# Optimization experiments

Measured on AMD Instinct MI355X. Metric: run time of the kernel, lower is better.

Reference implementation:

```python
import jax, jax.numpy as jnp
import numpy as np
import math

N_EMBD = 1024
N_HEAD = 16
HEAD_DIM = N_EMBD // N_HEAD
B, T = 2, 2048
LORA_RANK = 16      # 8-bit setting
LORA_SCALE = 32.0 / 16.0  # alpha / rank
QMIN, QMAX = 0.0, 255.0   # 8-bit asymmetric


def round_ste(x):
    return x + jax.lax.stop_gradient(jnp.round(x) - x)


def fake_quant(x, scale, zero_point):
    # LearnableFakeQuantize, asymmetric 8-bit, straight-through round
    q = jnp.clip(round_ste(x / scale + zero_point), QMIN, QMAX)
    return (q - zero_point) * scale


def lora_linear(x, w, b, la, lb):
    # base linear + LoRA path (dropout disabled / eval)
    return x @ w + b + LORA_SCALE * ((x @ la) @ lb)


def setup_inputs() -> dict:
    key = jax.random.key(0)
    ks = jax.random.split(key, 10)
    std = 0.02
    hidden_states = jax.random.normal(ks[0], (B, T, N_EMBD), dtype=jnp.float32)
    w_attn = jax.random.normal(ks[1], (N_EMBD, 3 * N_EMBD), dtype=jnp.float32) * std
    b_attn = jnp.zeros((3 * N_EMBD,), dtype=jnp.float32)
    la_attn = jax.random.normal(ks[2], (N_EMBD, LORA_RANK), dtype=jnp.float32) * std
    lb_attn = jnp.zeros((LORA_RANK, 3 * N_EMBD), dtype=jnp.float32)
    w_proj = jax.random.normal(ks[3], (N_EMBD, N_EMBD), dtype=jnp.float32) * std
    b_proj = jnp.zeros((N_EMBD,), dtype=jnp.float32)
    la_proj = jax.random.normal(ks[4], (N_EMBD, LORA_RANK), dtype=jnp.float32) * std
    lb_proj = jnp.zeros((LORA_RANK, N_EMBD), dtype=jnp.float32)
    kv_scale = jnp.asarray(0.05, dtype=jnp.float32)
    kv_zero_point = jnp.asarray(128.0, dtype=jnp.float32)
    return {
        'hidden_states': hidden_states,
        'w_attn': w_attn, 'b_attn': b_attn, 'la_attn': la_attn, 'lb_attn': lb_attn,
        'w_proj': w_proj, 'b_proj': b_proj, 'la_proj': la_proj, 'lb_proj': lb_proj,
        'kv_scale': kv_scale, 'kv_zero_point': kv_zero_point,
    }


def reference(hidden_states, w_attn, b_attn, la_attn, lb_attn,
              w_proj, b_proj, la_proj, lb_proj, kv_scale, kv_zero_point):
    Bn, Tn, C = hidden_states.shape
    qkv = lora_linear(hidden_states, w_attn, b_attn, la_attn, lb_attn)
    q, k, v = jnp.split(qkv, 3, axis=2)
    # [B, T, C] -> [B, H, T, D]
    def to_heads(x):
        return x.reshape(Bn, Tn, N_HEAD, HEAD_DIM).transpose(0, 2, 1, 3)
    q, k, v = to_heads(q), to_heads(k), to_heads(v)
    k = fake_quant(k, kv_scale, kv_zero_point)
    v = fake_quant(v, kv_scale, kv_zero_point)
    scores = jnp.einsum('bhqd,bhkd->bhqk', q, k) / math.sqrt(HEAD_DIM)
    causal = jnp.tril(jnp.ones((Tn, Tn), dtype=bool))
    scores = jnp.where(causal, scores, -jnp.inf)
    attn = jax.nn.softmax(scores, axis=-1)
    out = jnp.einsum('bhqk,bhkd->bhqd', attn, v)
    out = out.transpose(0, 2, 1, 3).reshape(Bn, Tn, C)
    return lora_linear(out, w_proj, b_proj, la_proj, lb_proj)
```

## Files before the change

kernel.cpp:

```cpp
#include <hip/hip_runtime.h>
#include <hip/hip_bf16.h>
#include <math.h>

#define N_EMBD   1024
#define N_HEAD   16
#define HEAD_DIM 64
#define BATCH    2
#define TSEQ     2048
#define RANK     16
#define LORA_SCALE 2.0f
#define M_TOTAL  (BATCH * TSEQ)
#define C3       (3 * N_EMBD)

typedef unsigned short ushort_t;
typedef __attribute__((ext_vector_type(8))) short bf16x8;
typedef __attribute__((ext_vector_type(4))) float f32x4;

__device__ __forceinline__ float fake_quant(float x, float scale, float zp) {
    float q = rintf(x / scale + zp);
    q = fminf(fmaxf(q, 0.0f), 255.0f);
    return (q - zp) * scale;
}

__device__ __forceinline__ ushort_t bf16bits(float f) {
    union { __hip_bfloat16 h; ushort_t u; } c;
    c.h = __float2bfloat16(f);
    return c.u;
}

__device__ __forceinline__ float bfraw2f(ushort_t u) {
    union { unsigned int i; float f; } c; c.i = ((unsigned int)u) << 16; return c.f;
}

#define NB_LORA 1024
#define NB_TRA  3072
#define NB_TRP  1024
#define NB_CVT  4096

__device__ __forceinline__ void transpose_body(
        const float* __restrict__ in, __hip_bfloat16* __restrict__ hiT,
        __hip_bfloat16* __restrict__ loT, int R, int C,
        int c0, int r0, int tid, float* sh) {
    float (*tl)[33] = (float(*)[33])sh;
    const int tx = tid & 31, ty = tid >> 5;
    for (int i = ty; i < 32; i += 8)
        tl[i][tx] = in[(size_t)(r0 + i) * C + c0 + tx];
    __syncthreads();
    for (int i = ty; i < 32; i += 8) {
        float v = tl[tx][i];
        __hip_bfloat16 h = __float2bfloat16(v);
        size_t o = (size_t)(c0 + i) * R + r0 + tx;
        hiT[o] = h;
        if (loT) loT[o] = __float2bfloat16(v - __bfloat162float(h));
    }
}

__global__ __launch_bounds__(256)
void prep_kernel(const float* __restrict__ x,
                 const float* __restrict__ w_attn,
                 const float* __restrict__ w_proj,
                 const float* __restrict__ la_attn,
                 __hip_bfloat16* __restrict__ x_hi,
                 __hip_bfloat16* __restrict__ x_lo,
                 __hip_bfloat16* __restrict__ wqT_h,
                 __hip_bfloat16* __restrict__ wqT_l,
                 __hip_bfloat16* __restrict__ wpT,
                 float* __restrict__ t_attn_p) {
    __shared__ float sh[33 * 32];
    const int tid = threadIdx.x;
    int b = blockIdx.x;

    if (b < NB_LORA) {
        const int bx = b & 255, by = b >> 8;
        float (*Xs)[64] = (float(*)[64])sh;
        const int ty = tid >> 4, tx = tid & 15;
        const int row0 = bx * 16;
        const int kbase = by * 256;
        float acc = 0.0f;
        for (int k0 = kbase; k0 < kbase + 256; k0 += 64) {
            int rr = tid >> 4, kk = (tid & 15) * 4;
            float4 v = *(const float4*)(x + (size_t)(row0 + rr) * N_EMBD + k0 + kk);
            Xs[rr][kk] = v.x; Xs[rr][kk + 1] = v.y; Xs[rr][kk + 2] = v.z; Xs[rr][kk + 3] = v.w;
            __syncthreads();
            for (int k = 0; k < 64; ++k)
                acc += Xs[ty][k] * la_attn[(size_t)(k0 + k) * RANK + tx];
            __syncthreads();
        }
        t_attn_p[((size_t)by * M_TOTAL + row0 + ty) * RANK + tx] = acc;
        return;
    }
    b -= NB_LORA;
    if (b < NB_TRA) {
        const int gx = b % (C3 / 32), gy = b / (C3 / 32);
        transpose_body(w_attn, wqT_h, wqT_l, N_EMBD, C3, gx * 32, gy * 32, tid, sh);
        return;
    }
    b -= NB_TRA;
    if (b < NB_TRP) {
        const int gx = b & 31, gy = b >> 5;
        transpose_body(w_proj, wpT, nullptr, N_EMBD, N_EMBD, gx * 32, gy * 32, tid, sh);
        return;
    }
    b -= NB_TRP;
    {
        const int i = b * 256 + tid;
        float4 v = ((const float4*)x)[i];
        float vs[4] = {v.x, v.y, v.z, v.w};
        #pragma unroll
        for (int k = 0; k < 4; ++k) {
            __hip_bfloat16 h = __float2bfloat16(vs[k]);
            x_hi[i * 4 + k] = h;
            x_lo[i * 4 + k] = __float2bfloat16(vs[k] - __bfloat162float(h));
        }
    }
}

__global__ void vtrans_kernel(const ushort_t* __restrict__ Vb,
                              ushort_t* __restrict__ Vt) {
    __shared__ ushort_t tl[64][68];
    const int bh = blockIdx.x & 31, tt = blockIdx.x >> 5;
    const int tid = threadIdx.x;
    {
        const int t = tid >> 2, d0 = (tid & 3) * 16;
        const uint4 u = *(const uint4*)(Vb + ((size_t)bh * TSEQ + tt * 64 + t) * 64 + d0);
        *(uint4*)&tl[t][d0] = u;
        *(uint4*)&tl[t][d0 + 8] = *(const uint4*)(Vb + ((size_t)bh * TSEQ + tt * 64 + t) * 64 + d0 + 8);
    }
    __syncthreads();
    const int d = tid >> 2, t0 = (tid & 3) * 16;
    unsigned int wbuf[8];
    #pragma unroll
    for (int j = 0; j < 8; ++j)
        wbuf[j] = (unsigned int)tl[t0 + 2 * j][d] | ((unsigned int)tl[t0 + 2 * j + 1][d] << 16);
    ushort_t* dst = Vt + ((size_t)bh * 64 + d) * TSEQ + tt * 64 + t0;
    *(uint4*)dst       = make_uint4(wbuf[0], wbuf[1], wbuf[2], wbuf[3]);
    *(uint4*)(dst + 8) = make_uint4(wbuf[4], wbuf[5], wbuf[6], wbuf[7]);
}

__global__ void lora_t_part_bf16_kernel(const ushort_t* __restrict__ x,
                                        const float* __restrict__ la,
                                        float* __restrict__ tpart, int K) {
    __shared__ float Xs[16][64];
    const int tid = threadIdx.x;
    const int ty = tid >> 4, tx = tid & 15;
    const int row0 = blockIdx.x * 16;
    const int kbase = blockIdx.y * 256;
    float acc = 0.0f;
    for (int k0 = kbase; k0 < kbase + 256; k0 += 64) {
        int rr = tid >> 4, kk = (tid & 15) * 4;
        const ushort4 u = *(const ushort4*)(x + (size_t)(row0 + rr) * K + k0 + kk);
        Xs[rr][kk] = bfraw2f(u.x); Xs[rr][kk + 1] = bfraw2f(u.y);
        Xs[rr][kk + 2] = bfraw2f(u.z); Xs[rr][kk + 3] = bfraw2f(u.w);
        __syncthreads();
        for (int k = 0; k < 64; ++k)
            acc += Xs[ty][k] * la[(size_t)(k0 + k) * RANK + tx];
        __syncthreads();
    }
    tpart[((size_t)blockIdx.y * M_TOTAL + row0 + ty) * RANK + tx] = acc;
}

__device__ __forceinline__ int sw_off(int r, int c) {
    return ((r >> 1) << 7) + (((((r & 1) << 2) | c) ^ ((r >> 1) & 7)) << 4);
}

template <bool SPLIT, int TM>
__global__ __launch_bounds__(256, 3)
void gemm_mfma_kernel(const __hip_bfloat16* __restrict__ Ah,
                      const __hip_bfloat16* __restrict__ Al,
                      const __hip_bfloat16* __restrict__ Bh,
                      const __hip_bfloat16* __restrict__ Bl,
                      const float* __restrict__ bias,
                      const float* __restrict__ tpart,
                      const float* __restrict__ lb,
                      float* __restrict__ Cf,
                      ushort_t* __restrict__ Qb,
                      ushort_t* __restrict__ Kb,
                      ushort_t* __restrict__ Vb,
                      const float* __restrict__ sp,
                      const float* __restrict__ zp,
                      int M, int N, int K, int split_col0, int out_mode) {
    constexpr int TILEA = TM * 32;
    constexpr int TILEB = 128 * 32;
    constexpr int MI = TM / 32;
    __shared__ __align__(16) __hip_bfloat16 As[3 * TILEA];
    __shared__ __align__(16) __hip_bfloat16 Bs[3 * TILEB];
    float* Ts = (float*)As;
    float* Ls = (float*)Bs;

    const int tid = threadIdx.x;
    const int lane = tid & 63, w = tid >> 6;

    int bcol, brow;
    {
        const int NC = gridDim.x, NR = gridDim.y;
        const int lid = blockIdx.y * NC + blockIdx.x;
        const int xcd = lid & 7, s = lid >> 3;
        const int cw = NC >> 1, rh = NR >> 2;
        const int cg = xcd & 1, rg = xcd >> 1;
        if (SPLIT) {
            bcol = 2 * (s % cw) + cg;
            brow = rg * rh + (s / cw);
        } else {
            bcol = cg * cw + (s % cw);
            brow = rg * rh + (s / cw);
        }
    }
    const int row0 = brow * TM, col0 = bcol * 128;
    const int wr = (w >> 1) * (TM >> 1), wc = (w & 1) * 64;
    const bool do_split = SPLIT && (col0 >= split_col0);

    const int s_lc = (lane & 7) ^ ((lane >> 3) & 7);
    const int s_rb = 2 * (lane >> 3) + (s_lc >> 2);
    const int s_c8 = (s_lc & 3) * 8;

    float qsc = 0.f, qzp = 0.f;
    if (out_mode == 1) { qsc = sp[0]; qzp = zp[0]; }

    f32x4 acc[MI][4];
    #pragma unroll
    for (int i = 0; i < MI; ++i)
        #pragma unroll
        for (int j = 0; j < 4; ++j)
            acc[i][j] = (f32x4){0.f, 0.f, 0.f, 0.f};

    const int arow = wr + (lane & 15);
    const int chunk = lane >> 4;

    const ushort_t* alp[MI];
    const ushort_t* blp[4];
    if (do_split) {
        #pragma unroll
        for (int mi = 0; mi < MI; ++mi)
            alp[mi] = (const ushort_t*)Al + (size_t)(row0 + arow + mi * 16) * K + chunk * 8;
        #pragma unroll
        for (int nj = 0; nj < 4; ++nj)
            blp[nj] = (const ushort_t*)Bl + (size_t)(col0 + wc + nj * 16 + (lane & 15)) * K + chunk * 8;
    }

    auto stage = [&](int buf, int kidx) {
        const int k0 = kidx << 5;
        __hip_bfloat16* dA = As + buf * TILEA;
        __hip_bfloat16* dB = Bs + buf * TILEB;
        if (TM == 128) {
            #pragma unroll
            for (int qq = 0; qq < 2; ++qq) {
                const int q = 2 * w + qq;
                const int r = 16 * q + s_rb;
                const __hip_bfloat16* gA = Ah + (size_t)(row0 + r) * K + k0 + s_c8;
                __builtin_amdgcn_global_load_lds(
                    (const __attribute__((address_space(1))) void*)gA,
                    (__attribute__((address_space(3))) void*)(dA + q * 512), 16, 0, 0);
                const __hip_bfloat16* gB = Bh + (size_t)(col0 + r) * K + k0 + s_c8;
                __builtin_amdgcn_global_load_lds(
                    (const __attribute__((address_space(1))) void*)gB,
                    (__attribute__((address_space(3))) void*)(dB + q * 512), 16, 0, 0);
            }
        } else {
            const int rA = 16 * w + s_rb;
            const __hip_bfloat16* gA = Ah + (size_t)(row0 + rA) * K + k0 + s_c8;
            __builtin_amdgcn_global_load_lds(
                (const __attribute__((address_space(1))) void*)gA,
                (__attribute__((address_space(3))) void*)(dA + w * 512), 16, 0, 0);
            #pragma unroll
            for (int qq = 0; qq < 2; ++qq) {
                const int q = 2 * w + qq;
                const int r = 16 * q + s_rb;
                const __hip_bfloat16* gB = Bh + (size_t)(col0 + r) * K + k0 + s_c8;
                __builtin_amdgcn_global_load_lds(
                    (const __attribute__((address_space(1))) void*)gB,
                    (__attribute__((address_space(3))) void*)(dB + q * 512), 16, 0, 0);
            }
        }
    };

    const int KI = K >> 5;
    stage(0, 0);
    stage(1, 1);
    int bcur = 0, bstage = 2;
    for (int kk = 0; kk < KI; ++kk) {
        if (kk == KI - 1) {
            asm volatile("s_waitcnt vmcnt(0)" ::: "memory");
        } else if (TM == 128) {
            asm volatile("s_waitcnt vmcnt(4)" ::: "memory");
        } else {
            asm volatile("s_waitcnt vmcnt(3)" ::: "memory");
        }
        __builtin_amdgcn_s_barrier();

        const int k0 = kk << 5;
        bf16x8 a_l[MI], b_l[4];
        if (do_split) {
            #pragma unroll
            for (int mi = 0; mi < MI; ++mi) a_l[mi] = *(const bf16x8*)(alp[mi] + k0);
            #pragma unroll
            for (int nj = 0; nj < 4; ++nj) b_l[nj] = *(const bf16x8*)(blp[nj] + k0);
        }
        if (kk + 2 < KI) { stage(bstage, kk + 2); bstage = (bstage == 2) ? 0 : bstage + 1; }

        const char* ab = (const char*)(As + bcur * TILEA);
        const char* bb = (const char*)(Bs + bcur * TILEB);
        bf16x8 a_h[MI], b_h[4];
        #pragma unroll
        for (int mi = 0; mi < MI; ++mi)
            a_h[mi] = *(const bf16x8*)(ab + sw_off(arow + mi * 16, chunk));
        #pragma unroll
        for (int nj = 0; nj < 4; ++nj)
            b_h[nj] = *(const bf16x8*)(bb + sw_off(wc + nj * 16 + (lane & 15), chunk));
        #pragma unroll
        for (int mi = 0; mi < MI; ++mi)
            #pragma unroll
            for (int nj = 0; nj < 4; ++nj)
                acc[mi][nj] = __builtin_amdgcn_mfma_f32_16x16x32_bf16(a_h[mi], b_h[nj], acc[mi][nj], 0, 0, 0);
        if (do_split) {
            #pragma unroll
            for (int mi = 0; mi < MI; ++mi)
                #pragma unroll
                for (int nj = 0; nj < 4; ++nj) {
                    acc[mi][nj] = __builtin_amdgcn_mfma_f32_16x16x32_bf16(a_h[mi], b_l[nj], acc[mi][nj], 0, 0, 0);
                    acc[mi][nj] = __builtin_amdgcn_mfma_f32_16x16x32_bf16(a_l[mi], b_h[nj], acc[mi][nj], 0, 0, 0);
                }
        }
        bcur = (bcur == 2) ? 0 : bcur + 1;
    }
    __syncthreads();

    {
        int r = tid >> 1, j0 = (tid & 1) * 8;
        if (r < TM) {
            float4 t0 = {0, 0, 0, 0}, t1 = {0, 0, 0, 0};
            #pragma unroll
            for (int c = 0; c < 4; ++c) {
                const float* src = tpart + ((size_t)c * M_TOTAL + row0 + r) * RANK + j0;
                float4 s0 = *(const float4*)src;
                float4 s1 = *(const float4*)(src + 4);
                t0.x += s0.x; t0.y += s0.y; t0.z += s0.z; t0.w += s0.w;
                t1.x += s1.x; t1.y += s1.y; t1.z += s1.z; t1.w += s1.w;
            }
            *(float4*)(Ts + r * 16 + j0)     = t0;
            *(float4*)(Ts + r * 16 + j0 + 4) = t1;
        }
        int rr = tid >> 4, c0 = (tid & 15) * 8;
        const float4* lsrc = (const float4*)(lb + (size_t)rr * N + col0 + c0);
        float4* ldst = (float4*)(Ls + rr * 128 + c0);
        ldst[0] = lsrc[0]; ldst[1] = lsrc[1];
    }
    __syncthreads();
    #pragma unroll
    for (int mi = 0; mi < MI; ++mi)
        #pragma unroll
        for (int nj = 0; nj < 4; ++nj) {
            const int coll = wc + nj * 16 + (lane & 15);
            const float bv = bias[col0 + coll];
            #pragma unroll
            for (int rg = 0; rg < 4; ++rg) {
                const int rowl = wr + mi * 16 + (lane >> 4) * 4 + rg;
                float lsum = 0.f;
                #pragma unroll
                for (int rr = 0; rr < 16; ++rr)
                    lsum += Ts[rowl * 16 + rr] * Ls[rr * 128 + coll];
                const float val = acc[mi][nj][rg] + bv + LORA_SCALE * lsum;
                if (out_mode == 0) {
                    Cf[(size_t)(row0 + rowl) * N + col0 + coll] = val;
                } else {
                    const int R = row0 + rowl;
                    const int b = R >> 11, t = R & 2047;
                    const int CN = col0 + coll;
                    const int sec = CN >> 10, head = (CN >> 6) & 15, d = CN & 63;
                    const size_t off = (((size_t)(b * 16 + head)) * TSEQ + t) * 64 + d;
                    if (sec == 0)      Qb[off] = bf16bits(val * 0.125f);
                    else if (sec == 1) Kb[off] = bf16bits(fake_quant(val, qsc, qzp));
                    else               Vb[off] = bf16bits(fake_quant(val, qsc, qzp));
                }
            }
        }
}

__global__ __launch_bounds__(256)
void mfma_attn_kernel(const ushort_t* __restrict__ Qb,
                      const ushort_t* __restrict__ Kq,
                      const ushort_t* __restrict__ Vtq,
                      ushort_t* __restrict__ outb) {
    const int bx = blockIdx.x;
    const int bh = bx & 31;
    const int qt = 31 - (bx >> 5);
    const int b = bh >> 4, h = bh & 15;
    const int tid = threadIdx.x;
    const int lane = tid & 63, w = tid >> 6;
    const int m16 = lane & 15, qc = lane >> 4;
    const int m7 = m16 & 7;

    __shared__ ushort_t Ks[2][4096];
    __shared__ ushort_t Vs[2][4096];
    __shared__ ushort_t Ps[4096];

    const int s_g = (lane & 7) ^ ((lane >> 3) & 7);
    const int s_r = lane >> 3;

    const ushort_t* Qg = Qb + (size_t)bh * TSEQ * 64;
    const ushort_t* Kg = Kq + (size_t)bh * TSEQ * 64;
    const ushort_t* Vg = Vtq + (size_t)bh * 64 * TSEQ;

    auto stageKV = [&](int buf, int kt) {
        #pragma unroll
        for (int pp = 0; pp < 2; ++pp) {
            const int p = 2 * w + pp;
            const ushort_t* gk = Kg + ((size_t)(kt * 64 + 8 * p + s_r)) * 64 + s_g * 8;
            __builtin_amdgcn_global_load_lds(
                (const __attribute__((address_space(1))) void*)gk,
                (__attribute__((address_space(3))) void*)(Ks[buf] + p * 512), 16, 0, 0);
            const ushort_t* gv = Vg + ((size_t)(8 * p + s_r)) * TSEQ + kt * 64 + s_g * 8;
            __builtin_amdgcn_global_load_lds(
                (const __attribute__((address_space(1))) void*)gv,
                (__attribute__((address_space(3))) void*)(Vs[buf] + p * 512), 16, 0, 0);
        }
    };

    stageKV(0, 0);

    bf16x8 a_q[2];
    {
        const ushort_t* qrow = Qg + (size_t)(qt * 64 + 16 * w + m16) * 64;
        a_q[0] = *(const bf16x8*)(qrow + qc * 8);
        a_q[1] = *(const bf16x8*)(qrow + (qc + 4) * 8);
    }

    float m_st[4], l_st[4];
    f32x4 o_acc[4];
    #pragma unroll
    for (int r = 0; r < 4; ++r) { m_st[r] = -INFINITY; l_st[r] = 0.0f; }
    #pragma unroll
    for (int dj = 0; dj < 4; ++dj) o_acc[dj] = (f32x4){0.f, 0.f, 0.f, 0.f};

    for (int kt = 0; kt <= qt; ++kt) {
        const int cur = kt & 1;
        if (kt < qt) {
            stageKV(cur ^ 1, kt + 1);
            asm volatile("s_waitcnt vmcnt(4)" ::: "memory");
        } else {
            asm volatile("s_waitcnt vmcnt(0)" ::: "memory");
        }
        __builtin_amdgcn_s_barrier();

        const bool diag = (kt == qt);
        const int nj_hi = diag ? (w + 1) : 4;

        f32x4 s[4];
        #pragma unroll
        for (int nj = 0; nj < 4; ++nj) s[nj] = (f32x4){0.f, 0.f, 0.f, 0.f};
        #pragma unroll
        for (int c = 0; c < 2; ++c) {
            #pragma unroll
            for (int nj = 0; nj < 4; ++nj) {
                if (nj < nj_hi) {
                    const int row = 16 * nj + m16;
                    const int g = qc + 4 * c;
                    bf16x8 bk = *(const bf16x8*)((const char*)Ks[cur] + row * 128 + ((g ^ m7) << 4));
                    s[nj] = __builtin_amdgcn_mfma_f32_16x16x32_bf16(a_q[c], bk, s[nj], 0, 0, 0);
                }
            }
        }

        float alpha[4], p_[4][4];
        #pragma unroll
        for (int reg = 0; reg < 4; ++reg) {
            const int qrow = 16 * w + 4 * qc + reg;
            float sv[4];
            float rm = -INFINITY;
            #pragma unroll
            for (int nj = 0; nj < 4; ++nj) {
                float v = s[nj][reg];
                if (diag && (m16 + 16 * nj > qrow)) v = -INFINITY;
                sv[nj] = v;
                rm = fmaxf(rm, v);
            }
            #pragma unroll
            for (int off = 1; off < 16; off <<= 1)
                rm = fmaxf(rm, __shfl_xor(rm, off, 16));
            const float mo = m_st[reg];
            const float mn = fmaxf(mo, rm);
            const float al = __expf(mo - mn);
            float rs = 0.f;
            #pragma unroll
            for (int nj = 0; nj < 4; ++nj) {
                float pv = __expf(sv[nj] - mn);
                p_[reg][nj] = pv;
                rs += pv;
            }
            #pragma unroll
            for (int off = 1; off < 16; off <<= 1)
                rs += __shfl_xor(rs, off, 16);
            l_st[reg] = al * l_st[reg] + rs;
            m_st[reg] = mn;
            alpha[reg] = al;
        }

        #pragma unroll
        for (int reg = 0; reg < 4; ++reg) {
            const int row = 16 * w + 4 * qc + reg;
            const int r7 = row & 7;
            #pragma unroll
            for (int nj = 0; nj < 4; ++nj) {
                const int k = m16 + 16 * nj;
                Ps[row * 64 + (((k >> 3) ^ r7) << 3) + (k & 7)] = bf16bits(p_[reg][nj]);
            }
        }

        #pragma unroll
        for (int dj = 0; dj < 4; ++dj)
            #pragma unroll
            for (int reg = 0; reg < 4; ++reg)
                o_acc[dj][reg] *= alpha[reg];

        const int c_hi = diag ? (w >= 2 ? 2 : 1) : 2;
        #pragma unroll
        for (int c = 0; c < 2; ++c) {
            if (c < c_hi) {
                const int rowp = 16 * w + m16;
                const int g = qc + 4 * c;
                bf16x8 ap = *(const bf16x8*)((const char*)Ps + rowp * 128 + ((g ^ m7) << 4));
                #pragma unroll
                for (int dj = 0; dj < 4; ++dj) {
                    const int rowv = 16 * dj + m16;
                    bf16x8 bv = *(const bf16x8*)((const char*)Vs[cur] + rowv * 128 + ((g ^ m7) << 4));
                    o_acc[dj] = __builtin_amdgcn_mfma_f32_16x16x32_bf16(ap, bv, o_acc[dj], 0, 0, 0);
                }
            }
        }
        asm volatile("s_barrier" ::: "memory");
    }

    #pragma unroll
    for (int reg = 0; reg < 4; ++reg) {
        const float inv = 1.0f / l_st[reg];
        const int q = qt * 64 + 16 * w + 4 * qc + reg;
        #pragma unroll
        for (int dj = 0; dj < 4; ++dj) {
            const int d = m16 + 16 * dj;
            outb[((size_t)b * TSEQ + q) * N_EMBD + h * 64 + d] = bf16bits(o_acc[dj][reg] * inv);
        }
    }
}

extern "C" void kernel_launch(void* const* d_in, const int* in_sizes, int n_in,
                              void* d_out, int out_size, void* d_ws, size_t ws_size,
                              hipStream_t stream) {
    const float* x        = (const float*)d_in[0];
    const float* w_attn   = (const float*)d_in[1];
    const float* b_attn   = (const float*)d_in[2];
    const float* la_attn  = (const float*)d_in[3];
    const float* lb_attn  = (const float*)d_in[4];
    const float* w_proj   = (const float*)d_in[5];
    const float* b_proj   = (const float*)d_in[6];
    const float* la_proj  = (const float*)d_in[7];
    const float* lb_proj  = (const float*)d_in[8];
    const float* kv_scale = (const float*)d_in[9];
    const float* kv_zp    = (const float*)d_in[10];
    float* out = (float*)d_out;

    char* ws = (char*)d_ws;
    float* t_attn_p       = (float*)ws;          ws += (size_t)4 * M_TOTAL * RANK * 4;
    float* t_proj_p       = (float*)ws;          ws += (size_t)4 * M_TOTAL * RANK * 4;
    ushort_t* aob         = (ushort_t*)ws;       ws += (size_t)M_TOTAL * N_EMBD * 2;
    __hip_bfloat16* x_hi  = (__hip_bfloat16*)ws; ws += (size_t)M_TOTAL * N_EMBD * 2;
    __hip_bfloat16* x_lo  = (__hip_bfloat16*)ws; ws += (size_t)M_TOTAL * N_EMBD * 2;
    __hip_bfloat16* wqT_h = (__hip_bfloat16*)ws; ws += (size_t)C3 * N_EMBD * 2;
    __hip_bfloat16* wqT_l = (__hip_bfloat16*)ws; ws += (size_t)C3 * N_EMBD * 2;
    __hip_bfloat16* wpT   = (__hip_bfloat16*)ws; ws += (size_t)N_EMBD * N_EMBD * 2;
    ushort_t* Qb          = (ushort_t*)ws;       ws += (size_t)32 * TSEQ * 64 * 2;
    ushort_t* Kb          = (ushort_t*)ws;       ws += (size_t)32 * TSEQ * 64 * 2;
    ushort_t* Vb          = (ushort_t*)ws;       ws += (size_t)32 * TSEQ * 64 * 2;
    ushort_t* Vtq         = (ushort_t*)ws;       ws += (size_t)32 * 64 * TSEQ * 2;

    prep_kernel<<<dim3(NB_LORA + NB_TRA + NB_TRP + NB_CVT), 256, 0, stream>>>(
        x, w_attn, w_proj, la_attn,
        x_hi, x_lo, wqT_h, wqT_l, wpT, t_attn_p);

    gemm_mfma_kernel<true, 128><<<dim3(24, 32), 256, 0, stream>>>(
        x_hi, x_lo, wqT_h, wqT_l, b_attn, t_attn_p, lb_attn,
        nullptr, Qb, Kb, Vb, kv_scale, kv_zp,
        M_TOTAL, C3, N_EMBD, 2 * N_EMBD, 1);

    vtrans_kernel<<<dim3(32 * (TSEQ / 64)), 256, 0, stream>>>(Vb, Vtq);

    mfma_attn_kernel<<<dim3(32 * 32), 256, 0, stream>>>(Qb, Kb, Vtq, aob);

    lora_t_part_bf16_kernel<<<dim3(M_TOTAL / 16, 4), 256, 0, stream>>>(aob, la_proj, t_proj_p, N_EMBD);

    gemm_mfma_kernel<false, 64><<<dim3(8, 64), 256, 0, stream>>>(
        (const __hip_bfloat16*)aob, nullptr, wpT, nullptr, b_proj, t_proj_p, lb_proj,
        out, nullptr, nullptr, nullptr, nullptr, nullptr,
        M_TOTAL, N_EMBD, N_EMBD, 1 << 30, 0);
}
```

Measured before the change: 297.6 us.

## Process two query tiles per attention block to reuse staged K/V

Each attention workgroup now handles two adjacent 64-row query tiles, sharing each double-buffered K/V tile load between them and keeping separate softmax state, accumulators and P buffers per tile. The grid is halved accordingly. This aims to cut global K/V traffic and staging overhead per query. It risks lower occupancy from more registers and LDS, and fewer, longer, more imbalanced blocks under the causal mask.

```diff
diff --git a/kernel.cpp b/kernel.cpp
--- a/kernel.cpp
+++ b/kernel.cpp
@@ -382,7 +382,8 @@
                       ushort_t* __restrict__ outb) {
     const int bx = blockIdx.x;
     const int bh = bx & 31;
-    const int qt = 31 - (bx >> 5);
+    const int pr = 15 - (bx >> 5);
+    const int qtA = 2 * pr, qtB = 2 * pr + 1;
     const int b = bh >> 4, h = bh & 15;
     const int tid = threadIdx.x;
     const int lane = tid & 63, w = tid >> 6;
@@ -391,7 +392,7 @@
 
     __shared__ ushort_t Ks[2][4096];
     __shared__ ushort_t Vs[2][4096];
-    __shared__ ushort_t Ps[4096];
+    __shared__ ushort_t Ps[8192];
 
     const int s_g = (lane & 7) ^ ((lane >> 3) & 7);
     const int s_r = lane >> 3;
@@ -417,23 +418,26 @@
 
     stageKV(0, 0);
 
-    bf16x8 a_q[2];
+    bf16x8 a_qA[2], a_qB[2];
     {
-        const ushort_t* qrow = Qg + (size_t)(qt * 64 + 16 * w + m16) * 64;
-        a_q[0] = *(const bf16x8*)(qrow + qc * 8);
-        a_q[1] = *(const bf16x8*)(qrow + (qc + 4) * 8);
-    }
-
-    float m_st[4], l_st[4];
-    f32x4 o_acc[4];
+        const ushort_t* qrA = Qg + (size_t)(qtA * 64 + 16 * w + m16) * 64;
+        a_qA[0] = *(const bf16x8*)(qrA + qc * 8);
+        a_qA[1] = *(const bf16x8*)(qrA + (qc + 4) * 8);
+        const ushort_t* qrB = Qg + (size_t)(qtB * 64 + 16 * w + m16) * 64;
+        a_qB[0] = *(const bf16x8*)(qrB + qc * 8);
+        a_qB[1] = *(const bf16x8*)(qrB + (qc + 4) * 8);
+    }
+
+    float mA[4], lA[4], mB[4], lB[4];
+    f32x4 oA[4], oB[4];
     #pragma unroll
-    for (int r = 0; r < 4; ++r) { m_st[r] = -INFINITY; l_st[r] = 0.0f; }
+    for (int r = 0; r < 4; ++r) { mA[r] = -INFINITY; lA[r] = 0.0f; mB[r] = -INFINITY; lB[r] = 0.0f; }
     #pragma unroll
-    for (int dj = 0; dj < 4; ++dj) o_acc[dj] = (f32x4){0.f, 0.f, 0.f, 0.f};
-
-    for (int kt = 0; kt <= qt; ++kt) {
+    for (int dj = 0; dj < 4; ++dj) { oA[dj] = (f32x4){0.f, 0.f, 0.f, 0.f}; oB[dj] = (f32x4){0.f, 0.f, 0.f, 0.f}; }
+
+    for (int kt = 0; kt <= qtB; ++kt) {
         const int cur = kt & 1;
-        if (kt < qt) {
+        if (kt < qtB) {
             stageKV(cur ^ 1, kt + 1);
             asm volatile("s_waitcnt vmcnt(4)" ::: "memory");
         } else {
@@ -441,88 +445,168 @@
         }
         __builtin_amdgcn_s_barrier();
 
-        const bool diag = (kt == qt);
-        const int nj_hi = diag ? (w + 1) : 4;
-
-        f32x4 s[4];
-        #pragma unroll
-        for (int nj = 0; nj < 4; ++nj) s[nj] = (f32x4){0.f, 0.f, 0.f, 0.f};
-        #pragma unroll
-        for (int c = 0; c < 2; ++c) {
-            #pragma unroll
-            for (int nj = 0; nj < 4; ++nj) {
-                if (nj < nj_hi) {
-                    const int row = 16 * nj + m16;
+        if (kt <= qtA) {
+            const bool diag = (kt == qtA);
+            const int nj_hi = diag ? (w + 1) : 4;
+            f32x4 s[4];
+            #pragma unroll
+            for (int nj = 0; nj < 4; ++nj) s[nj] = (f32x4){0.f, 0.f, 0.f, 0.f};
+            #pragma unroll
+            for (int c = 0; c < 2; ++c) {
+                #pragma unroll
+                for (int nj = 0; nj < 4; ++nj) {
+                    if (nj < nj_hi) {
+                        const int row = 16 * nj + m16;
+                        const int g = qc + 4 * c;
+                        bf16x8 bk = *(const bf16x8*)((const char*)Ks[cur] + row * 128 + ((g ^ m7) << 4));
+                        s[nj] = __builtin_amdgcn_mfma_f32_16x16x32_bf16(a_qA[c], bk, s[nj], 0, 0, 0);
+                    }
+                }
+            }
+            float alpha[4], p_[4][4];
+            #pragma unroll
+            for (int reg = 0; reg < 4; ++reg) {
+                const int qrow = 16 * w + 4 * qc + reg;
+                float sv[4];
+                float rm = -INFINITY;
+                #pragma unroll
+                for (int nj = 0; nj < 4; ++nj) {
+                    float v = s[nj][reg];
+                    if (diag && (m16 + 16 * nj > qrow)) v = -INFINITY;
+                    sv[nj] = v;
+                    rm = fmaxf(rm, v);
+                }
+                #pragma unroll
+                for (int off = 1; off < 16; off <<= 1)
+                    rm = fmaxf(rm, __shfl_xor(rm, off, 16));
+                const float mo = mA[reg];
+                const float mn = fmaxf(mo, rm);
+                const float al = __expf(mo - mn);
+                float rs = 0.f;
+                #pragma unroll
+                for (int nj = 0; nj < 4; ++nj) {
+                    float pv = __expf(sv[nj] - mn);
+                    p_[reg][nj] = pv;
+                    rs += pv;
+                }
+                #pragma unroll
+                for (int off = 1; off < 16; off <<= 1)
+                    rs += __shfl_xor(rs, off, 16);
+                lA[reg] = al * lA[reg] + rs;
+                mA[reg] = mn;
+                alpha[reg] = al;
+            }
+            #pragma unroll
+            for (int reg = 0; reg < 4; ++reg) {
+                const int row = 16 * w + 4 * qc + reg;
+                const int r7 = row & 7;
+                #pragma unroll
+                for (int nj = 0; nj < 4; ++nj) {
+                    const int k = m16 + 16 * nj;
+                    Ps[row * 64 + (((k >> 3) ^ r7) << 3) + (k & 7)] = bf16bits(p_[reg][nj]);
+                }
+            }
+            #pragma unroll
+            for (int dj = 0; dj < 4; ++dj)
+                #pragma unroll
+                for (int reg = 0; reg < 4; ++reg)
+                    oA[dj][reg] *= alpha[reg];
+            const int c_hi = diag ? (w >= 2 ? 2 : 1) : 2;
+            #pragma unroll
+            for (int c = 0; c < 2; ++c) {
+                if (c < c_hi) {
+                    const int rowp = 16 * w + m16;
                     const int g = qc + 4 * c;
-                    bf16x8 bk = *(const bf16x8*)((const char*)Ks[cur] + row * 128 + ((g ^ m7) << 4));
-                    s[nj] = __builtin_amdgcn_mfma_f32_16x16x32_bf16(a_q[c], bk, s[nj], 0, 0, 0);
-                }
-            }
-        }
-
-        float alpha[4], p_[4][4];
-        #pragma unroll
-        for (int reg = 0; reg < 4; ++reg) {
-            const int qrow = 16 * w + 4 * qc + reg;
-            float sv[4];
-            float rm = -INFINITY;
-            #pragma unroll
-            for (int nj = 0; nj < 4; ++nj) {
-                float v = s[nj][reg];
-                if (diag && (m16 + 16 * nj > qrow)) v = -INFINITY;
-                sv[nj] = v;
-                rm = fmaxf(rm, v);
-            }
-            #pragma unroll
-            for (int off = 1; off < 16; off <<= 1)
-                rm = fmaxf(rm, __shfl_xor(rm, off, 16));
-            const float mo = m_st[reg];
-            const float mn = fmaxf(mo, rm);
-            const float al = __expf(mo - mn);
-            float rs = 0.f;
-            #pragma unroll
-            for (int nj = 0; nj < 4; ++nj) {
-                float pv = __expf(sv[nj] - mn);
-                p_[reg][nj] = pv;
-                rs += pv;
-            }
-            #pragma unroll
-            for (int off = 1; off < 16; off <<= 1)
-                rs += __shfl_xor(rs, off, 16);
-            l_st[reg] = al * l_st[reg] + rs;
-            m_st[reg] = mn;
-            alpha[reg] = al;
-        }
-
-        #pragma unroll
-        for (int reg = 0; reg < 4; ++reg) {
-            const int row = 16 * w + 4 * qc + reg;
-            const int r7 = row & 7;
-            #pragma unroll
-            for (int nj = 0; nj < 4; ++nj) {
-                const int k = m16 + 16 * nj;
-                Ps[row * 64 + (((k >> 3) ^ r7) << 3) + (k & 7)] = bf16bits(p_[reg][nj]);
-            }
-        }
-
-        #pragma unroll
-        for (int dj = 0; dj < 4; ++dj)
-            #pragma unroll
-            for (int reg = 0; reg < 4; ++reg)
-                o_acc[dj][reg] *= alpha[reg];
-
-        const int c_hi = diag ? (w >= 2 ? 2 : 1) : 2;
-        #pragma unroll
-        for (int c = 0; c < 2; ++c) {
-            if (c < c_hi) {
-                const int rowp = 16 * w + m16;
-                const int g = qc + 4 * c;
-                bf16x8 ap = *(const bf16x8*)((const char*)Ps + rowp * 128 + ((g ^ m7) << 4));
-                #pragma unroll
-                for (int dj = 0; dj < 4; ++dj) {
-                    const int rowv = 16 * dj + m16;
-                    bf16x8 bv = *(const bf16x8*)((const char*)Vs[cur] + rowv * 128 + ((g ^ m7) << 4));
-                    o_acc[dj] = __builtin_amdgcn_mfma_f32_16x16x32_bf16(ap, bv, o_acc[dj], 0, 0, 0);
+                    bf16x8 ap = *(const bf16x8*)((const char*)Ps + rowp * 128 + ((g ^ m7) << 4));
+                    #pragma unroll
+                    for (int dj = 0; dj < 4; ++dj) {
+                        const int rowv = 16 * dj + m16;
+                        bf16x8 bv = *(const bf16x8*)((const char*)Vs[cur] + rowv * 128 + ((g ^ m7) << 4));
+                        oA[dj] = __builtin_amdgcn_mfma_f32_16x16x32_bf16(ap, bv, oA[dj], 0, 0, 0);
+                    }
+                }
+            }
+        }
+
+        {
+            const bool diag = (kt == qtB);
+            const int nj_hi = diag ? (w + 1) : 4;
+            f32x4 s[4];
+            #pragma unroll
+            for (int nj = 0; nj < 4; ++nj) s[nj] = (f32x4){0.f, 0.f, 0.f, 0.f};
+            #pragma unroll
+            for (int c = 0; c < 2; ++c) {
+                #pragma unroll
+                for (int nj = 0; nj < 4; ++nj) {
+                    if (nj < nj_hi) {
+                        const int row = 16 * nj + m16;
+                        const int g = qc + 4 * c;
+                        bf16x8 bk = *(const bf16x8*)((const char*)Ks[cur] + row * 128 + ((g ^ m7) << 4));
+                        s[nj] = __builtin_amdgcn_mfma_f32_16x16x32_bf16(a_qB[c], bk, s[nj], 0, 0, 0);
+                    }
+                }
+            }
+            float alpha[4], p_[4][4];
+            #pragma unroll
+            for (int reg = 0; reg < 4; ++reg) {
+                const int qrow = 16 * w + 4 * qc + reg;
+                float sv[4];
+                float rm = -INFINITY;
+                #pragma unroll
+                for (int nj = 0; nj < 4; ++nj) {
+                    float v = s[nj][reg];
+                    if (diag && (m16 + 16 * nj > qrow)) v = -INFINITY;
+                    sv[nj] = v;
+                    rm = fmaxf(rm, v);
+                }
+                #pragma unroll
+                for (int off = 1; off < 16; off <<= 1)
+                    rm = fmaxf(rm, __shfl_xor(rm, off, 16));
+                const float mo = mB[reg];
+                const float mn = fmaxf(mo, rm);
+                const float al = __expf(mo - mn);
+                float rs = 0.f;
+                #pragma unroll
+                for (int nj = 0; nj < 4; ++nj) {
+                    float pv = __expf(sv[nj] - mn);
+                    p_[reg][nj] = pv;
+                    rs += pv;
+                }
+                #pragma unroll
+                for (int off = 1; off < 16; off <<= 1)
+                    rs += __shfl_xor(rs, off, 16);
+                lB[reg] = al * lB[reg] + rs;
+                mB[reg] = mn;
+                alpha[reg] = al;
+            }
+            #pragma unroll
+            for (int reg = 0; reg < 4; ++reg) {
+                const int row = 16 * w + 4 * qc + reg;
+                const int r7 = row & 7;
+                #pragma unroll
+                for (int nj = 0; nj < 4; ++nj) {
+                    const int k = m16 + 16 * nj;
+                    Ps[4096 + row * 64 + (((k >> 3) ^ r7) << 3) + (k & 7)] = bf16bits(p_[reg][nj]);
+                }
+            }
+            #pragma unroll
+            for (int dj = 0; dj < 4; ++dj)
+                #pragma unroll
+                for (int reg = 0; reg < 4; ++reg)
+                    oB[dj][reg] *= alpha[reg];
+            const int c_hi = diag ? (w >= 2 ? 2 : 1) : 2;
+            #pragma unroll
+            for (int c = 0; c < 2; ++c) {
+                if (c < c_hi) {
+                    const int rowp = 16 * w + m16;
+                    const int g = qc + 4 * c;
+                    bf16x8 ap = *(const bf16x8*)((const char*)Ps + 8192 + rowp * 128 + ((g ^ m7) << 4));
+                    #pragma unroll
+                    for (int dj = 0; dj < 4; ++dj) {
+                        const int rowv = 16 * dj + m16;
+                        bf16x8 bv = *(const bf16x8*)((const char*)Vs[cur] + rowv * 128 + ((g ^ m7) << 4));
+                        oB[dj] = __builtin_amdgcn_mfma_f32_16x16x32_bf16(ap, bv, oB[dj], 0, 0, 0);
+                    }
                 }
             }
         }
@@ -531,12 +615,15 @@
 
     #pragma unroll
     for (int reg = 0; reg < 4; ++reg) {
-        const float inv = 1.0f / l_st[reg];
-        const int q = qt * 64 + 16 * w + 4 * qc + reg;
+        const float invA = 1.0f / lA[reg];
+        const int qA = qtA * 64 + 16 * w + 4 * qc + reg;
+        const float invB = 1.0f / lB[reg];
+        const int qB = qtB * 64 + 16 * w + 4 * qc + reg;
         #pragma unroll
         for (int dj = 0; dj < 4; ++dj) {
             const int d = m16 + 16 * dj;
-            outb[((size_t)b * TSEQ + q) * N_EMBD + h * 64 + d] = bf16bits(o_acc[dj][reg] * inv);
+            outb[((size_t)b * TSEQ + qA) * N_EMBD + h * 64 + d] = bf16bits(oA[dj][reg] * invA);
+            outb[((size_t)b * TSEQ + qB) * N_EMBD + h * 64 + d] = bf16bits(oB[dj][reg] * invB);
         }
     }
 }
@@ -582,7 +669,7 @@
 
     vtrans_kernel<<<dim3(32 * (TSEQ / 64)), 256, 0, stream>>>(Vb, Vtq);
 
-    mfma_attn_kernel<<<dim3(32 * 32), 256, 0, stream>>>(Qb, Kb, Vtq, aob);
+    mfma_attn_kernel<<<dim3(16 * 32), 256, 0, stream>>>(Qb, Kb, Vtq, aob);
 
     lora_t_part_bf16_kernel<<<dim3(M_TOTAL / 16, 4), 256, 0, stream>>>(aob, la_proj, t_proj_p, N_EMBD);
 
```

New measurement: 341.6 us. 14.8% more time.
